# Optimization experiments

Measured on AMD Instinct MI355X. Metric: run time of the kernel, lower is better.

The kernel has to match this reference:

```python
import jax, jax.numpy as jnp
import numpy as np

N_QUBITS = 12
LAYERS = 4
ENCODERS = ['angle_rx', 'angle_ry', 'h_angle_rx', 'h_angle_ry']

_INV_SQRT2 = 1.0 / np.sqrt(2.0)
H_GATE = jnp.array([[_INV_SQRT2, _INV_SQRT2], [_INV_SQRT2, -_INV_SQRT2]], dtype=jnp.complex64)


def rx_mat(t):
    # t: scalar or (B,) -> (...,2,2)
    c = jnp.cos(t / 2).astype(jnp.complex64)
    s = jnp.sin(t / 2).astype(jnp.complex64)
    return jnp.stack([jnp.stack([c, -1j * s], -1), jnp.stack([-1j * s, c], -1)], -2)


def ry_mat(t):
    c = jnp.cos(t / 2).astype(jnp.complex64)
    s = jnp.sin(t / 2).astype(jnp.complex64)
    return jnp.stack([jnp.stack([c, -s], -1), jnp.stack([s, c], -1)], -2)


def rz_mat(t):
    e = jnp.exp(-1j * t.astype(jnp.complex64) / 2)
    z = jnp.zeros_like(e)
    return jnp.stack([jnp.stack([e, z], -1), jnp.stack([z, jnp.conj(e)], -1)], -2)


def apply_1q(state, U, q, n):
    # state: (B, 2^n); wire q is axis q in big-endian (PennyLane) ordering
    B = state.shape[0]
    L, R = 2 ** q, 2 ** (n - q - 1)
    s = state.reshape(B, L, 2, R)
    if U.ndim == 2:
        s = jnp.einsum('ab,BLbR->BLaR', U, s)
    else:  # per-sample gate (B,2,2)
        s = jnp.einsum('Bab,BLbR->BLaR', U, s)
    return s.reshape(B, 2 ** n)


def apply_cnot_adjacent(state, q, n):
    # CNOT(control=q, target=q+1)
    B = state.shape[0]
    L, R = 2 ** q, 2 ** (n - q - 2)
    s = state.reshape(B, L, 2, 2, R)
    s = jnp.stack([s[:, :, 0], s[:, :, 1, ::-1]], axis=2)
    return s.reshape(B, 2 ** n)


def run_circuit(features, theta, encoder, n, layers):
    B = features.shape[0]
    state = jnp.zeros((B, 2 ** n), dtype=jnp.complex64).at[:, 0].set(1.0)
    use_h = encoder.startswith('h_')
    rot = rx_mat if encoder.endswith('rx') else ry_mat
    # encoding: one angle per qubit, batched gate
    for q in range(n):
        if use_h:
            state = apply_1q(state, H_GATE, q, n)
        state = apply_1q(state, rot(features[:, q]), q, n)
    # variational block (hadamard=False)
    for l in range(layers):
        for q in range(n):
            state = apply_1q(state, rx_mat(theta[l, q, 0]), q, n)
            state = apply_1q(state, ry_mat(theta[l, q, 1]), q, n)
            state = apply_1q(state, rz_mat(theta[l, q, 2]), q, n)
        for q in range(0, n - 1, 2):
            state = apply_cnot_adjacent(state, q, n)
        for q in range(1, n - 1, 2):
            state = apply_cnot_adjacent(state, q, n)
    # <Z_q> for every qubit
    p = jnp.abs(state) ** 2  # (B, 2^n)
    ez = []
    for q in range(n):
        pr = p.reshape(B, 2 ** q, 2, -1)
        ez.append(pr[:, :, 0].sum((1, 2)) - pr[:, :, 1].sum((1, 2)))
    return jnp.stack(ez, axis=-1)  # (B, n)


def setup_inputs() -> dict:
    key = jax.random.key(0)
    k1, k2 = jax.random.split(key)
    features = jax.random.uniform(k1, (1024, N_QUBITS), dtype=jnp.float32)
    theta = 0.01 * jax.random.normal(k2, (LAYERS, N_QUBITS, 3), dtype=jnp.float32)
    alpha = jnp.zeros((len(ENCODERS),), dtype=jnp.float32)
    return {"features": features, "theta": theta, "alpha": alpha}


def reference(features, theta, alpha):
    arch_w = jax.nn.softmax(alpha)
    branch = jnp.stack(
        [run_circuit(features, theta, enc, N_QUBITS, LAYERS) for enc in ENCODERS], axis=0
    )  # (E, B, n_qubits)
    y = jnp.einsum('e,ebq->bq', arch_w, branch)
    return y
```

## Files before the change

### kernel.cpp

```cpp
#include <hip/hip_runtime.h>
#include <math.h>

#define NQ 12
#define DIM 4096
#define NL 4
#define THREADS 256

typedef float v2f __attribute__((ext_vector_type(2)));

#define SWZC(e) ((e) ^ (((e) >> 3) & 14) ^ (((e) >> 7) & 15))

__device__ __forceinline__ v2f pkfma(v2f a, v2f b, v2f c) {
    v2f d; asm("v_pk_fma_f32 %0, %1, %2, %3" : "=v"(d) : "v"(a), "v"(b), "v"(c)); return d;
}
__device__ __forceinline__ v2f pkmul(v2f a, v2f b) {
    v2f d; asm("v_pk_mul_f32 %0, %1, %2" : "=v"(d) : "v"(a), "v"(b)); return d;
}
__device__ __forceinline__ v2f pkadd(v2f a, v2f b) {
    v2f d; asm("v_pk_add_f32 %0, %1, %2" : "=v"(d) : "v"(a), "v"(b)); return d;
}

__device__ __forceinline__ float2 cmulS(float2 a, float2 b) {
    return make_float2(fmaf(a.x, b.x, -a.y * b.y), fmaf(a.x, b.y, a.y * b.x));
}

struct C3 { v2f r, i, ni; };

#define CMULP(orE, orI, K, xre, xim) \
    { orE = pkfma(K.ni, xim, pkmul(K.r, xre)); orI = pkfma(K.i, xre, pkmul(K.r, xim)); }
#define CMACP(orE, orI, K, xre, xim) \
    { orE = pkfma(K.r, xre, pkfma(K.ni, xim, orE)); orI = pkfma(K.r, xim, pkfma(K.i, xre, orI)); }

#define QUADBODY(A_, B_, C_, D_) { \
    v2f z0r,z0i,z1r,z1i,z2r,z2i,z3r,z3i; \
    CMULP(z0r,z0i, l00, sre[A_], sim[A_]); CMACP(z0r,z0i, l01, sre[B_], sim[B_]); \
    CMULP(z1r,z1i, l10, sre[A_], sim[A_]); CMACP(z1r,z1i, l11, sre[B_], sim[B_]); \
    CMULP(z2r,z2i, l00, sre[C_], sim[C_]); CMACP(z2r,z2i, l01, sre[D_], sim[D_]); \
    CMULP(z3r,z3i, l10, sre[C_], sim[C_]); CMACP(z3r,z3i, l11, sre[D_], sim[D_]); \
    v2f y0r,y0i,y1r,y1i,y2r,y2i,y3r,y3i; \
    CMULP(y0r,y0i, h00, z0r,z0i); CMACP(y0r,y0i, h01, z2r,z2i); \
    CMULP(y1r,y1i, h00, z1r,z1i); CMACP(y1r,y1i, h01, z3r,z3i); \
    CMULP(y2r,y2i, h10, z0r,z0i); CMACP(y2r,y2i, h11, z2r,z2i); \
    CMULP(y3r,y3i, h10, z1r,z1i); CMACP(y3r,y3i, h11, z3r,z3i); \
    sre[A_]=y0r; sim[A_]=y0i; sre[B_]=y1r; sim[B_]=y1i; \
    sre[C_]=y3r; sim[C_]=y3i; sre[D_]=y2r; sim[D_]=y2i; }

#define LOADU \
    C3 l00={U[0][0],U[0][1],U[0][2]}, l01={U[1][0],U[1][1],U[1][2]}, \
       l10={U[2][0],U[2][1],U[2][2]}, l11={U[3][0],U[3][1],U[3][2]}, \
       h00={U[4][0],U[4][1],U[4][2]}, h01={U[5][0],U[5][1],U[5][2]}, \
       h10={U[6][0],U[6][1],U[6][2]}, h11={U[7][0],U[7][1],U[7][2]};

__device__ __forceinline__ void pass_hi(v2f* sre, v2f* sim, const v2f (*U)[3]) {
    LOADU
    QUADBODY(0,4,8,12) QUADBODY(1,5,9,13) QUADBODY(2,6,10,14) QUADBODY(3,7,11,15)
}
__device__ __forceinline__ void pass_lo(v2f* sre, v2f* sim, const v2f (*U)[3]) {
    LOADU
    QUADBODY(0,1,2,3) QUADBODY(4,5,6,7) QUADBODY(8,9,10,11) QUADBODY(12,13,14,15)
}

__global__ __launch_bounds__(THREADS, 2)
void vqc_kernel(const float* __restrict__ features,
                const float* __restrict__ theta,
                const float* __restrict__ alpha,
                float* __restrict__ out)
{
    __shared__ v2f re_p[DIM];
    __shared__ v2f im_p[DIM];
    __shared__ float2 cs[NL * NQ * 3];
    __shared__ float2 U48[NL * NQ][4];
    __shared__ v2f Upk[24][8][3];
    __shared__ float2 enc[2][NQ][2];
    __shared__ float2 pairT[2][6][4];
    __shared__ float2 loc[2][16];
    __shared__ v2f red[12 * 4];
    __shared__ float wez[12];

    const int tid = threadIdx.x;
    const bool special = (blockIdx.x == 0);
    const int gA = special ? 0 : 2 * ((int)blockIdx.x - 1);
    const int gB = gA + 1;

    if (tid < NL * NQ * 3) {
        float s, c; sincosf(0.5f * theta[tid], &s, &c);
        cs[tid] = make_float2(c, s);
    }
    if (tid >= 160 && tid < 184) {
        int c_ = (tid - 160) / 12, q = (tid - 160) % 12;
        const float r_ = 0.70710678118654752f;
        float2 a0, a1;
        if (special) { a0 = make_float2(r_, 0.f); a1 = a0; }
        else {
            int g = c_ ? gB : gA;
            int esl = g % 3, b = g / 3;
            float f = features[b * NQ + q];
            float s, c; sincosf(0.5f * f, &s, &c);
            if (esl == 0)      { a0 = make_float2(c, 0.f); a1 = make_float2(0.f, -s); }
            else if (esl == 1) { a0 = make_float2(c, 0.f); a1 = make_float2(s, 0.f); }
            else               { a0 = make_float2((c-s)*r_, 0.f); a1 = make_float2((c+s)*r_, 0.f); }
        }
        enc[c_][q][0] = a0; enc[c_][q][1] = a1;
    }
    __syncthreads();

    if (tid < NL * NQ) {
        float c0 = cs[tid*3+0].x, s0 = cs[tid*3+0].y;
        float c1 = cs[tid*3+1].x, s1 = cs[tid*3+1].y;
        float c2 = cs[tid*3+2].x, s2 = cs[tid*3+2].y;
        float2 a00 = make_float2( c1*c0,  s1*s0);
        float2 a01 = make_float2(-s1*c0, -c1*s0);
        float2 a10 = make_float2( s1*c0, -c1*s0);
        float2 a11 = make_float2( c1*c0, -s1*s0);
        float2 ep = make_float2(c2, -s2), em = make_float2(c2, s2);
        U48[tid][0] = cmulS(ep, a00); U48[tid][1] = cmulS(ep, a01);
        U48[tid][2] = cmulS(em, a10); U48[tid][3] = cmulS(em, a11);
    }
    if (tid >= 64 && tid < 112) {
        int x = tid - 64;
        int c_ = x / 24, y = x % 24, p = y >> 2, v = y & 3;
        pairT[c_][p][v] = cmulS(enc[c_][2*p][v >> 1], enc[c_][2*p + 1][v & 1]);
    }
    __syncthreads();

    if (tid < 192) {
        int p = tid >> 3, k = tid & 7;
        int l = p / 6, m = p % 6;
        int q = (k < 4) ? (2*m + 1) : (2*m);
        float2 u = U48[l*NQ + q][k & 3];
        v2f r2 = {u.x, u.x}, i2 = {u.y, u.y}, n2 = {-u.y, -u.y};
        Upk[p][k][0] = r2; Upk[p][k][1] = i2; Upk[p][k][2] = n2;
    }
    if (tid >= 192 && tid < 224) {
        int x = tid - 192; int c_ = x >> 4, j = x & 15;
        loc[c_][j] = cmulS(pairT[c_][4][j >> 2], pairT[c_][5][j & 3]);
    }
    __syncthreads();

    v2f sre[16], sim[16];
    {
        int t = tid;
        float2 preA = cmulS(cmulS(pairT[0][0][(t>>6)&3], pairT[0][1][(t>>4)&3]),
                            cmulS(pairT[0][2][(t>>2)&3], pairT[0][3][t&3]));
        float2 preB = cmulS(cmulS(pairT[1][0][(t>>6)&3], pairT[1][1][(t>>4)&3]),
                            cmulS(pairT[1][2][(t>>2)&3], pairT[1][3][t&3]));
        #pragma unroll
        for (int j = 0; j < 16; ++j) {
            float2 aA = cmulS(preA, loc[0][j]);
            float2 aB = cmulS(preB, loc[1][j]);
            v2f r = {aA.x, aB.x}, i = {aA.y, aB.y};
            sre[j] = r; sim[j] = i;
        }
    }

    #pragma unroll 1
    for (int l = 0; l < NL; ++l) {
        pass_hi(sre, sim, Upk[l*6 + 4]);
        pass_lo(sre, sim, Upk[l*6 + 5]);
        {
            int ba = SWZC(tid << 4);
            #pragma unroll
            for (int j = 0; j < 16; ++j) { re_p[ba ^ j] = sre[j]; im_p[ba ^ j] = sim[j]; }
            __syncthreads();
            int ib = ((tid >> 4) << 8) | (tid & 15);
            int bb = SWZC(ib);
            #pragma unroll
            for (int j = 0; j < 16; ++j) { int a = bb ^ SWZC(j << 4); sre[j] = re_p[a]; sim[j] = im_p[a]; }
            __syncthreads();
        }
        pass_hi(sre, sim, Upk[l*6 + 2]);
        pass_lo(sre, sim, Upk[l*6 + 3]);
        {
            int ib = ((tid >> 4) << 8) | (tid & 15);
            int bb = SWZC(ib);
            #pragma unroll
            for (int j = 0; j < 16; ++j) { int a = bb ^ SWZC(j << 4); re_p[a] = sre[j]; im_p[a] = sim[j]; }
            __syncthreads();
            int bc = SWZC(tid);
            #pragma unroll
            for (int j = 0; j < 16; ++j) { int a = bc ^ SWZC(j << 8); sre[j] = re_p[a]; sim[j] = im_p[a]; }
            __syncthreads();
        }
        pass_hi(sre, sim, Upk[l*6 + 0]);
        pass_lo(sre, sim, Upk[l*6 + 1]);
        if (l < NL - 1) {
            int bc = SWZC(tid);
            #pragma unroll
            for (int j = 0; j < 16; ++j) { int a = bc ^ SWZC(j << 8); re_p[a] = sre[j]; im_p[a] = sim[j]; }
            __syncthreads();
            int t = tid;
            int sx = (t << 4) ^ ((t & 1) << 3) ^ (((t >> 2) & 1) << 5)
                             ^ (((t >> 4) & 1) << 7) ^ (((t >> 6) & 1) << 9);
            int bs = SWZC(sx);
            #pragma unroll
            for (int j = 0; j < 16; ++j) {
                int sj = j ^ ((j >> 1) & 2);
                sre[j] = re_p[bs ^ sj]; sim[j] = im_p[bs ^ sj];
            }
            __syncthreads();
        }
    }

    v2f s0 = {0.f,0.f}, s1 = {0.f,0.f}, s2 = {0.f,0.f}, s3 = {0.f,0.f}, psum = {0.f,0.f};
    {
        const v2f MONE = {-1.f, -1.f};
        #pragma unroll
        for (int j = 0; j < 16; ++j) {
            v2f p = pkfma(sim[j], sim[j], pkmul(sre[j], sre[j]));
            psum = pkadd(psum, p);
            if (j & 8)                        s0 = pkfma(p, MONE, s0); else s0 = pkadd(s0, p);
            if (j & 4)                        s1 = pkfma(p, MONE, s1); else s1 = pkadd(s1, p);
            if ((((j >> 1) ^ (j >> 2)) & 1))  s2 = pkfma(p, MONE, s2); else s2 = pkadd(s2, p);
            if (j & 1)                        s3 = pkfma(p, MONE, s3); else s3 = pkadd(s3, p);
        }
    }
    v2f vals[12];
    {
        int t = tid;
        int mt = t ^ ((t >> 1) & 0xAA);
        vals[0] = s0; vals[1] = s1; vals[2] = s2; vals[3] = s3;
        vals[4]  = ((t >> 7) & 1)  ? -s3 : s3;
        vals[5]  = ((mt >> 6) & 1) ? -psum : psum;
        vals[6]  = ((mt >> 5) & 1) ? -psum : psum;
        vals[7]  = ((mt >> 4) & 1) ? -psum : psum;
        vals[8]  = ((mt >> 3) & 1) ? -psum : psum;
        vals[9]  = ((mt >> 2) & 1) ? -psum : psum;
        vals[10] = ((mt >> 1) & 1) ? -psum : psum;
        vals[11] = (mt & 1)        ? -psum : psum;
    }
    const int lane = tid & 63, wv = tid >> 6;
    #pragma unroll
    for (int q = 0; q < 12; ++q) {
        v2f v = vals[q];
        #pragma unroll
        for (int mm = 32; mm >= 1; mm >>= 1) {
            v.x += __shfl_xor(v.x, mm, 64);
            v.y += __shfl_xor(v.y, mm, 64);
        }
        if (lane == 0) red[q * 4 + wv] = v;
    }
    __syncthreads();

    if (tid < 12) {
        v2f v = pkadd(pkadd(red[tid*4+0], red[tid*4+1]), pkadd(red[tid*4+2], red[tid*4+3]));
        float A0 = alpha[0], A1 = alpha[1], A2 = alpha[2], A3 = alpha[3];
        float mx = fmaxf(fmaxf(A0, A1), fmaxf(A2, A3));
        float E0 = expf(A0-mx), E1 = expf(A1-mx), E2 = expf(A2-mx), E3 = expf(A3-mx);
        float den = E0 + E1 + E2 + E3;
        if (special) {
            wez[tid] = (E2 / den) * v.x;
        } else {
            int eslA = gA % 3, bA = gA / 3;
            int eslB = gB % 3, bB = gB / 3;
            float wA = ((eslA == 0) ? E0 : (eslA == 1) ? E1 : E3) / den;
            float wB = ((eslB == 0) ? E0 : (eslB == 1) ? E1 : E3) / den;
            atomicAdd(out + bA * NQ + tid, wA * v.x);
            atomicAdd(out + bB * NQ + tid, wB * v.y);
        }
    }
    if (special) {
        __syncthreads();
        for (int bb2 = tid; bb2 < 1024; bb2 += THREADS) {
            #pragma unroll
            for (int q = 0; q < NQ; ++q)
                atomicAdd(out + bb2 * NQ + q, wez[q]);
        }
    }
}

extern "C" void kernel_launch(void* const* d_in, const int* in_sizes, int n_in,
                              void* d_out, int out_size, void* d_ws, size_t ws_size,
                              hipStream_t stream) {
    const float* features = (const float*)d_in[0];
    const float* theta    = (const float*)d_in[1];
    const float* alpha    = (const float*)d_in[2];
    float* out = (float*)d_out;

    hipMemsetAsync(out, 0, (size_t)out_size * sizeof(float), stream);
    vqc_kernel<<<dim3(1537), THREADS, 0, stream>>>(features, theta, alpha, out);
}
```

Measured before the change: 144.5 us.

## Halve LDS footprint, exploit unitary gate structure, use wave-local fences for intra-wave transposes

The state transposes now run through a single shared scratch buffer, moving real and imaginary parts in sequence. Setup tables alias into that same buffer to shrink LDS use, and launch bounds target 4 blocks per CU instead of 2. The fused 2x2 gate constants exploit the SU(2) structure, storing 2 entries with 4 sign variants instead of 4 entries with 3, which cuts shared-memory reads and register pressure. The first transpose stays within a wavefront, so its block barriers become wave barriers. Splitting re/im doubles the number of barriers in the other transposes, and the higher occupancy target may force register spilling.

```diff
diff --git a/kernel.cpp b/kernel.cpp
--- a/kernel.cpp
+++ b/kernel.cpp
@@ -5,10 +5,10 @@
 #define DIM 4096
 #define NL 4
 #define THREADS 256
+#define SWZC(e) ((e) ^ (((e) >> 3) & 14) ^ (((e) >> 7) & 15))
+#define WAVEFENCE() { __builtin_amdgcn_wave_barrier(); __builtin_amdgcn_sched_barrier(0); }
 
 typedef float v2f __attribute__((ext_vector_type(2)));
-
-#define SWZC(e) ((e) ^ (((e) >> 3) & 14) ^ (((e) >> 7) & 15))
 
 __device__ __forceinline__ v2f pkfma(v2f a, v2f b, v2f c) {
     v2f d; asm("v_pk_fma_f32 %0, %1, %2, %3" : "=v"(d) : "v"(a), "v"(b), "v"(c)); return d;
@@ -19,63 +19,58 @@
 __device__ __forceinline__ v2f pkadd(v2f a, v2f b) {
     v2f d; asm("v_pk_add_f32 %0, %1, %2" : "=v"(d) : "v"(a), "v"(b)); return d;
 }
-
 __device__ __forceinline__ float2 cmulS(float2 a, float2 b) {
     return make_float2(fmaf(a.x, b.x, -a.y * b.y), fmaf(a.x, b.y, a.y * b.x));
 }
 
-struct C3 { v2f r, i, ni; };
-
-#define CMULP(orE, orI, K, xre, xim) \
-    { orE = pkfma(K.ni, xim, pkmul(K.r, xre)); orI = pkfma(K.i, xre, pkmul(K.r, xim)); }
-#define CMACP(orE, orI, K, xre, xim) \
-    { orE = pkfma(K.r, xre, pkfma(K.ni, xim, orE)); orI = pkfma(K.r, xim, pkfma(K.i, xre, orI)); }
+struct C4 { v2f r, i, ni, nr; };
+
+#define CMUL4(orE, orI, KR, KNI, KI, xre, xim) \
+    { orE = pkfma(KNI, xim, pkmul(KR, xre)); orI = pkfma(KI, xre, pkmul(KR, xim)); }
+#define CMAC4(orE, orI, KR, KNI, KI, xre, xim) \
+    { orE = pkfma(KR, xre, pkfma(KNI, xim, orE)); orI = pkfma(KR, xim, pkfma(KI, xre, orI)); }
 
 #define QUADBODY(A_, B_, C_, D_) { \
     v2f z0r,z0i,z1r,z1i,z2r,z2i,z3r,z3i; \
-    CMULP(z0r,z0i, l00, sre[A_], sim[A_]); CMACP(z0r,z0i, l01, sre[B_], sim[B_]); \
-    CMULP(z1r,z1i, l10, sre[A_], sim[A_]); CMACP(z1r,z1i, l11, sre[B_], sim[B_]); \
-    CMULP(z2r,z2i, l00, sre[C_], sim[C_]); CMACP(z2r,z2i, l01, sre[D_], sim[D_]); \
-    CMULP(z3r,z3i, l10, sre[C_], sim[C_]); CMACP(z3r,z3i, l11, sre[D_], sim[D_]); \
+    CMUL4(z0r,z0i, la.r, la.ni, la.i, sre[A_], sim[A_]); CMAC4(z0r,z0i, lb.r, lb.ni, lb.i, sre[B_], sim[B_]); \
+    CMUL4(z1r,z1i, lb.nr, lb.ni, lb.i, sre[A_], sim[A_]); CMAC4(z1r,z1i, la.r, la.i, la.ni, sre[B_], sim[B_]); \
+    CMUL4(z2r,z2i, la.r, la.ni, la.i, sre[C_], sim[C_]); CMAC4(z2r,z2i, lb.r, lb.ni, lb.i, sre[D_], sim[D_]); \
+    CMUL4(z3r,z3i, lb.nr, lb.ni, lb.i, sre[C_], sim[C_]); CMAC4(z3r,z3i, la.r, la.i, la.ni, sre[D_], sim[D_]); \
     v2f y0r,y0i,y1r,y1i,y2r,y2i,y3r,y3i; \
-    CMULP(y0r,y0i, h00, z0r,z0i); CMACP(y0r,y0i, h01, z2r,z2i); \
-    CMULP(y1r,y1i, h00, z1r,z1i); CMACP(y1r,y1i, h01, z3r,z3i); \
-    CMULP(y2r,y2i, h10, z0r,z0i); CMACP(y2r,y2i, h11, z2r,z2i); \
-    CMULP(y3r,y3i, h10, z1r,z1i); CMACP(y3r,y3i, h11, z3r,z3i); \
+    CMUL4(y0r,y0i, ha.r, ha.ni, ha.i, z0r, z0i); CMAC4(y0r,y0i, hb.r, hb.ni, hb.i, z2r, z2i); \
+    CMUL4(y1r,y1i, ha.r, ha.ni, ha.i, z1r, z1i); CMAC4(y1r,y1i, hb.r, hb.ni, hb.i, z3r, z3i); \
+    CMUL4(y2r,y2i, hb.nr, hb.ni, hb.i, z0r, z0i); CMAC4(y2r,y2i, ha.r, ha.i, ha.ni, z2r, z2i); \
+    CMUL4(y3r,y3i, hb.nr, hb.ni, hb.i, z1r, z1i); CMAC4(y3r,y3i, ha.r, ha.i, ha.ni, z3r, z3i); \
     sre[A_]=y0r; sim[A_]=y0i; sre[B_]=y1r; sim[B_]=y1i; \
     sre[C_]=y3r; sim[C_]=y3i; sre[D_]=y2r; sim[D_]=y2i; }
 
-#define LOADU \
-    C3 l00={U[0][0],U[0][1],U[0][2]}, l01={U[1][0],U[1][1],U[1][2]}, \
-       l10={U[2][0],U[2][1],U[2][2]}, l11={U[3][0],U[3][1],U[3][2]}, \
-       h00={U[4][0],U[4][1],U[4][2]}, h01={U[5][0],U[5][1],U[5][2]}, \
-       h10={U[6][0],U[6][1],U[6][2]}, h11={U[7][0],U[7][1],U[7][2]};
-
-__device__ __forceinline__ void pass_hi(v2f* sre, v2f* sim, const v2f (*U)[3]) {
-    LOADU
+__device__ __forceinline__ void pass_hi(v2f* sre, v2f* sim, const v2f (*U)[4]) {
+    C4 la={U[0][0],U[0][1],U[0][2],U[0][3]}, lb={U[1][0],U[1][1],U[1][2],U[1][3]},
+       ha={U[2][0],U[2][1],U[2][2],U[2][3]}, hb={U[3][0],U[3][1],U[3][2],U[3][3]};
     QUADBODY(0,4,8,12) QUADBODY(1,5,9,13) QUADBODY(2,6,10,14) QUADBODY(3,7,11,15)
 }
-__device__ __forceinline__ void pass_lo(v2f* sre, v2f* sim, const v2f (*U)[3]) {
-    LOADU
+__device__ __forceinline__ void pass_lo(v2f* sre, v2f* sim, const v2f (*U)[4]) {
+    C4 la={U[0][0],U[0][1],U[0][2],U[0][3]}, lb={U[1][0],U[1][1],U[1][2],U[1][3]},
+       ha={U[2][0],U[2][1],U[2][2],U[2][3]}, hb={U[3][0],U[3][1],U[3][2],U[3][3]};
     QUADBODY(0,1,2,3) QUADBODY(4,5,6,7) QUADBODY(8,9,10,11) QUADBODY(12,13,14,15)
 }
 
-__global__ __launch_bounds__(THREADS, 2)
+__global__ __launch_bounds__(THREADS, 4)
 void vqc_kernel(const float* __restrict__ features,
                 const float* __restrict__ theta,
                 const float* __restrict__ alpha,
                 float* __restrict__ out)
 {
-    __shared__ v2f re_p[DIM];
-    __shared__ v2f im_p[DIM];
-    __shared__ float2 cs[NL * NQ * 3];
-    __shared__ float2 U48[NL * NQ][4];
-    __shared__ v2f Upk[24][8][3];
-    __shared__ float2 enc[2][NQ][2];
-    __shared__ float2 pairT[2][6][4];
-    __shared__ float2 loc[2][16];
+    __shared__ v2f scr[DIM];
+    __shared__ v2f Upk[24][4][4];
     __shared__ v2f red[12 * 4];
     __shared__ float wez[12];
+
+    float2* cs = (float2*)scr;
+    float2 (*U48)[4] = (float2(*)[4])((char*)scr + 1152);
+    float2 (*enc)[2] = (float2(*)[2])((char*)scr + 2688);
+    float2 (*pairT)[4] = (float2(*)[4])((char*)scr + 3072);
+    float2* loc = (float2*)((char*)scr + 3456);
 
     const int tid = threadIdx.x;
     const bool special = (blockIdx.x == 0);
@@ -100,7 +95,7 @@
             else if (esl == 1) { a0 = make_float2(c, 0.f); a1 = make_float2(s, 0.f); }
             else               { a0 = make_float2((c-s)*r_, 0.f); a1 = make_float2((c+s)*r_, 0.f); }
         }
-        enc[c_][q][0] = a0; enc[c_][q][1] = a1;
+        enc[c_ * NQ + q][0] = a0; enc[c_ * NQ + q][1] = a1;
     }
     __syncthreads();
 
@@ -119,39 +114,41 @@
     if (tid >= 64 && tid < 112) {
         int x = tid - 64;
         int c_ = x / 24, y = x % 24, p = y >> 2, v = y & 3;
-        pairT[c_][p][v] = cmulS(enc[c_][2*p][v >> 1], enc[c_][2*p + 1][v & 1]);
-    }
-    __syncthreads();
-
-    if (tid < 192) {
-        int p = tid >> 3, k = tid & 7;
+        pairT[c_ * 6 + p][v] = cmulS(enc[c_*NQ + 2*p][v >> 1], enc[c_*NQ + 2*p + 1][v & 1]);
+    }
+    __syncthreads();
+
+    for (int idx = tid; idx < 384; idx += THREADS) {
+        int p = idx >> 4, rest = idx & 15, c = rest >> 2, comp = rest & 3;
         int l = p / 6, m = p % 6;
-        int q = (k < 4) ? (2*m + 1) : (2*m);
-        float2 u = U48[l*NQ + q][k & 3];
-        v2f r2 = {u.x, u.x}, i2 = {u.y, u.y}, n2 = {-u.y, -u.y};
-        Upk[p][k][0] = r2; Upk[p][k][1] = i2; Upk[p][k][2] = n2;
+        int q = (c < 2) ? (2*m + 1) : (2*m);
+        float2 u = U48[l*NQ + q][c & 1];
+        float xv = (comp == 0) ? u.x : (comp == 1) ? u.y : (comp == 2) ? -u.y : -u.x;
+        v2f vv = {xv, xv};
+        Upk[p][c][comp] = vv;
     }
     if (tid >= 192 && tid < 224) {
         int x = tid - 192; int c_ = x >> 4, j = x & 15;
-        loc[c_][j] = cmulS(pairT[c_][4][j >> 2], pairT[c_][5][j & 3]);
+        loc[c_ * 16 + j] = cmulS(pairT[c_*6 + 4][j >> 2], pairT[c_*6 + 5][j & 3]);
     }
     __syncthreads();
 
     v2f sre[16], sim[16];
     {
         int t = tid;
-        float2 preA = cmulS(cmulS(pairT[0][0][(t>>6)&3], pairT[0][1][(t>>4)&3]),
-                            cmulS(pairT[0][2][(t>>2)&3], pairT[0][3][t&3]));
-        float2 preB = cmulS(cmulS(pairT[1][0][(t>>6)&3], pairT[1][1][(t>>4)&3]),
-                            cmulS(pairT[1][2][(t>>2)&3], pairT[1][3][t&3]));
+        float2 preA = cmulS(cmulS(pairT[0][(t>>6)&3], pairT[1][(t>>4)&3]),
+                            cmulS(pairT[2][(t>>2)&3], pairT[3][t&3]));
+        float2 preB = cmulS(cmulS(pairT[6][(t>>6)&3], pairT[7][(t>>4)&3]),
+                            cmulS(pairT[8][(t>>2)&3], pairT[9][t&3]));
         #pragma unroll
         for (int j = 0; j < 16; ++j) {
-            float2 aA = cmulS(preA, loc[0][j]);
-            float2 aB = cmulS(preB, loc[1][j]);
-            v2f r = {aA.x, aB.x}, i = {aA.y, aB.y};
-            sre[j] = r; sim[j] = i;
-        }
-    }
+            float2 aA = cmulS(preA, loc[j]);
+            float2 aB = cmulS(preB, loc[16 + j]);
+            v2f r = {aA.x, aB.x}, ii = {aA.y, aB.y};
+            sre[j] = r; sim[j] = ii;
+        }
+    }
+    __syncthreads();
 
     #pragma unroll 1
     for (int l = 0; l < NL; ++l) {
@@ -159,45 +156,60 @@
         pass_lo(sre, sim, Upk[l*6 + 5]);
         {
             int ba = SWZC(tid << 4);
-            #pragma unroll
-            for (int j = 0; j < 16; ++j) { re_p[ba ^ j] = sre[j]; im_p[ba ^ j] = sim[j]; }
-            __syncthreads();
             int ib = ((tid >> 4) << 8) | (tid & 15);
             int bb = SWZC(ib);
             #pragma unroll
-            for (int j = 0; j < 16; ++j) { int a = bb ^ SWZC(j << 4); sre[j] = re_p[a]; sim[j] = im_p[a]; }
-            __syncthreads();
+            for (int j = 0; j < 16; ++j) scr[ba ^ j] = sre[j];
+            WAVEFENCE();
+            #pragma unroll
+            for (int j = 0; j < 16; ++j) sre[j] = scr[bb ^ SWZC(j << 4)];
+            WAVEFENCE();
+            #pragma unroll
+            for (int j = 0; j < 16; ++j) scr[ba ^ j] = sim[j];
+            WAVEFENCE();
+            #pragma unroll
+            for (int j = 0; j < 16; ++j) sim[j] = scr[bb ^ SWZC(j << 4)];
+            WAVEFENCE();
         }
         pass_hi(sre, sim, Upk[l*6 + 2]);
         pass_lo(sre, sim, Upk[l*6 + 3]);
         {
             int ib = ((tid >> 4) << 8) | (tid & 15);
             int bb = SWZC(ib);
-            #pragma unroll
-            for (int j = 0; j < 16; ++j) { int a = bb ^ SWZC(j << 4); re_p[a] = sre[j]; im_p[a] = sim[j]; }
-            __syncthreads();
             int bc = SWZC(tid);
             #pragma unroll
-            for (int j = 0; j < 16; ++j) { int a = bc ^ SWZC(j << 8); sre[j] = re_p[a]; sim[j] = im_p[a]; }
+            for (int j = 0; j < 16; ++j) scr[bb ^ SWZC(j << 4)] = sre[j];
+            __syncthreads();
+            #pragma unroll
+            for (int j = 0; j < 16; ++j) sre[j] = scr[bc ^ SWZC(j << 8)];
+            __syncthreads();
+            #pragma unroll
+            for (int j = 0; j < 16; ++j) scr[bb ^ SWZC(j << 4)] = sim[j];
+            __syncthreads();
+            #pragma unroll
+            for (int j = 0; j < 16; ++j) sim[j] = scr[bc ^ SWZC(j << 8)];
             __syncthreads();
         }
         pass_hi(sre, sim, Upk[l*6 + 0]);
         pass_lo(sre, sim, Upk[l*6 + 1]);
         if (l < NL - 1) {
             int bc = SWZC(tid);
-            #pragma unroll
-            for (int j = 0; j < 16; ++j) { int a = bc ^ SWZC(j << 8); re_p[a] = sre[j]; im_p[a] = sim[j]; }
-            __syncthreads();
             int t = tid;
             int sx = (t << 4) ^ ((t & 1) << 3) ^ (((t >> 2) & 1) << 5)
                              ^ (((t >> 4) & 1) << 7) ^ (((t >> 6) & 1) << 9);
             int bs = SWZC(sx);
             #pragma unroll
-            for (int j = 0; j < 16; ++j) {
-                int sj = j ^ ((j >> 1) & 2);
-                sre[j] = re_p[bs ^ sj]; sim[j] = im_p[bs ^ sj];
-            }
-            __syncthreads();
+            for (int j = 0; j < 16; ++j) scr[bc ^ SWZC(j << 8)] = sre[j];
+            __syncthreads();
+            #pragma unroll
+            for (int j = 0; j < 16; ++j) { int sj = j ^ ((j >> 1) & 2); sre[j] = scr[bs ^ sj]; }
+            __syncthreads();
+            #pragma unroll
+            for (int j = 0; j < 16; ++j) scr[bc ^ SWZC(j << 8)] = sim[j];
+            __syncthreads();
+            #pragma unroll
+            for (int j = 0; j < 16; ++j) { int sj = j ^ ((j >> 1) & 2); sim[j] = scr[bs ^ sj]; }
+            WAVEFENCE();
         }
     }
 
```

Result: faster. 134.9 us (-6.7%).
